# Kernel optimization log

Measured on AMD Instinct MI355X. Metric: run time of the kernel, lower is better.

## Reference

```python
import jax, jax.numpy as jnp
import numpy as np

N_NODES = 200000
N_EDGES = 6400000
N_GRAPHS = 1024
N_EMB = 1032
D = 16


def _gcn_conv(x, W, b, src, dst, n):
    # PyG GCNConv: h = x W; symmetric norm with self-loops; aggregate onto target (dst)
    h = x @ W
    deg = jax.ops.segment_sum(jnp.ones_like(dst, dtype=h.dtype), dst, num_segments=n) + 1.0
    dis = jax.lax.rsqrt(deg)
    norm = dis[src] * dis[dst]                      # [E]
    agg = jax.ops.segment_sum(h[src] * norm[:, None], dst, num_segments=n)
    agg = agg + h * (dis * dis)[:, None]            # self-loop term
    return agg + b


def _protein_embed(ids, edge_index, batch_ids, emb, W1, b1, W2, b2):
    n = ids.shape[0]
    x = emb[ids]                                    # embedding lookup [N, D]
    src, dst = edge_index[0], edge_index[1]
    h = jax.nn.relu(_gcn_conv(x, W1, b1, src, dst, n))
    h = _gcn_conv(h, W2, b2, src, dst, n)
    # global_mean_pool over graphs
    sums = jax.ops.segment_sum(h, batch_ids, num_segments=N_GRAPHS)
    cnt = jax.ops.segment_sum(jnp.ones((n,), h.dtype), batch_ids, num_segments=N_GRAPHS)
    return sums / jnp.maximum(cnt, 1.0)[:, None]    # [B, D]


def setup_inputs() -> dict:
    key = jax.random.key(0)
    ks = jax.random.split(key, 10)
    emb = jax.random.normal(ks[0], (N_EMB, D), jnp.float32) * 0.1
    W1 = jax.random.normal(ks[1], (D, D), jnp.float32) * (1.0 / np.sqrt(D))
    W2 = jax.random.normal(ks[2], (D, D), jnp.float32) * (1.0 / np.sqrt(D))
    fcW = jax.random.normal(ks[3], (6, 2 * D), jnp.float32) * (1.0 / np.sqrt(2 * D))
    b1 = jnp.zeros((D,), jnp.float32)
    b2 = jnp.zeros((D,), jnp.float32)
    fcb = jnp.zeros((6,), jnp.float32)
    rx = jax.random.randint(ks[4], (N_NODES,), 0, N_EMB)
    r_edge_index = jax.random.randint(ks[5], (2, N_EDGES), 0, N_NODES)
    r_batch = jnp.sort(jax.random.randint(ks[6], (N_NODES,), 0, N_GRAPHS))
    lx = jax.random.randint(ks[7], (N_NODES,), 0, N_EMB)
    l_edge_index = jax.random.randint(ks[8], (2, N_EDGES), 0, N_NODES)
    l_batch = jnp.sort(jax.random.randint(ks[9], (N_NODES,), 0, N_GRAPHS))
    return {"emb": emb, "W1": W1, "b1": b1, "W2": W2, "b2": b2, "fcW": fcW, "fcb": fcb,
            "rx": rx, "r_edge_index": r_edge_index, "r_batch": r_batch,
            "lx": lx, "l_edge_index": l_edge_index, "l_batch": l_batch}


def reference(emb, W1, b1, W2, b2, fcW, fcb, rx, r_edge_index, r_batch, lx, l_edge_index, l_batch):
    r = _protein_embed(rx, r_edge_index, r_batch, emb, W1, b1, W2, b2)
    l = _protein_embed(lx, l_edge_index, l_batch, emb, W1, b1, W2, b2)
    h = jnp.concatenate([r, l], axis=1)             # [B, 2D]
    out = h @ fcW.T + fcb                           # [B, 6]
    return out[:, :3], out[:, 3:]
```

## Files before the change

kernel.cpp:

```cpp
#include <hip/hip_runtime.h>
#include <hip/hip_bf16.h>

#define N_NODES 200000
#define N_GRAPHS 1024
#define D 16
#define NEDGE 6400000

#define BNODES 256
#define NBUK 782
#define NCH 512
#define ECHUNK 12500
#define EC4 (ECHUNK / 4)
#define OSTRIDE (NBUK + 1)
#define CAP 9216
#define GBLK 12500
#define GHALF 6250

__global__ __launch_bounds__(1024) void pA(
        const int* __restrict__ srcR, const int* __restrict__ dstR,
        const int* __restrict__ srcL, const int* __restrict__ dstL,
        unsigned int* __restrict__ slabC_R, unsigned int* __restrict__ slabC_L,
        int* __restrict__ offsT_R, int* __restrict__ offsT_L) {
    const int* src = blockIdx.y ? srcL : srcR;
    const int* dst = blockIdx.y ? dstL : dstR;
    unsigned int* slabC = blockIdx.y ? slabC_L : slabC_R;
    int* offsT = blockIdx.y ? offsT_L : offsT_R;

    __shared__ unsigned int stage[ECHUNK];
    __shared__ int lh[NBUK];
    __shared__ int lcur[NBUK];
    __shared__ int wsum[16];
    int t = threadIdx.x;
    int wave = t >> 6, lane = t & 63;
    int c = blockIdx.x;
    int base = c * ECHUNK;
    const int4* dst4 = (const int4*)(dst + base);
    const int4* src4 = (const int4*)(src + base);

    for (int k = t; k < NBUK; k += 1024) lh[k] = 0;
    __syncthreads();
    for (int i = t; i < EC4; i += 1024) {
        int4 d4 = dst4[i];
        atomicAdd(&lh[((unsigned int)d4.x) >> 8], 1);
        atomicAdd(&lh[((unsigned int)d4.y) >> 8], 1);
        atomicAdd(&lh[((unsigned int)d4.z) >> 8], 1);
        atomicAdd(&lh[((unsigned int)d4.w) >> 8], 1);
    }
    __syncthreads();

    int v = (t < NBUK) ? lh[t] : 0;
    int x = v;
#pragma unroll
    for (int d0 = 1; d0 < 64; d0 <<= 1) {
        int y = __shfl_up(x, d0, 64);
        if (lane >= d0) x += y;
    }
    if (lane == 63) wsum[wave] = x;
    __syncthreads();
    if (wave == 0 && lane < 16) {
        int s = wsum[lane];
#pragma unroll
        for (int d0 = 1; d0 < 16; d0 <<= 1) {
            int y = __shfl_up(s, d0, 64);
            if (lane >= d0) s += y;
        }
        wsum[lane] = s;
    }
    __syncthreads();
    int excl = x - v + (wave ? wsum[wave - 1] : 0);
    if (t < NBUK) lcur[t] = excl;
    __syncthreads();

    for (int i = t; i < EC4; i += 1024) {
        int4 d4 = dst4[i];
        int4 s4 = src4[i];
        int dd[4] = {d4.x, d4.y, d4.z, d4.w};
        int ss[4] = {s4.x, s4.y, s4.z, s4.w};
#pragma unroll
        for (int k = 0; k < 4; k++) {
            int pos = atomicAdd(&lcur[dd[k] >> 8], 1);
            stage[pos] = ((unsigned int)(dd[k] & 255) << 18) | (unsigned int)ss[k];
        }
    }
    __syncthreads();
    uint4* out4 = (uint4*)(slabC + base);
    const uint4* st4 = (const uint4*)stage;
    for (int i = t; i < EC4; i += 1024) out4[i] = st4[i];
    if (t < NBUK) offsT[c * OSTRIDE + t] = excl;
    if (t == 0) offsT[c * OSTRIDE + NBUK] = ECHUNK;
}

__global__ __launch_bounds__(256) void tr_kernel(
        const int* __restrict__ offsT_R, const int* __restrict__ offsT_L,
        int* __restrict__ offsTT_R, int* __restrict__ offsTT_L) {
    const int* in = blockIdx.z ? offsT_L : offsT_R;
    int* outp = blockIdx.z ? offsTT_L : offsTT_R;
    __shared__ int tile[32][33];
    int lx = threadIdx.x & 31, ly = threadIdx.x >> 5;
#pragma unroll
    for (int r = 0; r < 32; r += 8) {
        int row = blockIdx.y * 32 + ly + r;
        int col = blockIdx.x * 32 + lx;
        if (col < OSTRIDE) tile[ly + r][lx] = in[row * OSTRIDE + col];
    }
    __syncthreads();
#pragma unroll
    for (int r = 0; r < 32; r += 8) {
        int orow = blockIdx.x * 32 + ly + r;
        int ocol = blockIdx.y * 32 + lx;
        if (orow < OSTRIDE) outp[orow * NCH + ocol] = tile[lx][ly + r];
    }
}

__global__ __launch_bounds__(256) void pB(
        const unsigned int* __restrict__ slabC_R, const unsigned int* __restrict__ slabC_L,
        const int* __restrict__ offsTT_R, const int* __restrict__ offsTT_L,
        unsigned int* __restrict__ slabR, unsigned int* __restrict__ slabL,
        int2* __restrict__ metaR, int2* __restrict__ metaL,
        float* __restrict__ disR, float* __restrict__ disL) {
    int y = blockIdx.y;
    const unsigned int* slabC = y ? slabC_L : slabC_R;
    const int* offsTT = y ? offsTT_L : offsTT_R;
    unsigned int* slab = y ? slabL : slabR;
    int2* meta = y ? metaL : metaR;
    float* dis = y ? disL : disR;

    __shared__ unsigned int sin_[CAP];
    __shared__ int hcnt[BNODES], hoff[BNODES], hcur[BNODES];
    __shared__ int wtot[4];
    __shared__ int totc;
    int t = threadIdx.x;
    int lane = t & 63, wave = t >> 6;
    int b = blockIdx.x;

    int a0 = offsTT[b * NCH + t],        e0 = offsTT[(b + 1) * NCH + t];
    int a1 = offsTT[b * NCH + t + 256],  e1 = offsTT[(b + 1) * NCH + t + 256];
    int len = (e0 - a0) + (e1 - a1);

    int x = len;
#pragma unroll
    for (int d0 = 1; d0 < 64; d0 <<= 1) {
        int yy = __shfl_up(x, d0, 64);
        if (lane >= d0) x += yy;
    }
    if (lane == 63) wtot[wave] = x;
    hcnt[t] = 0;
    __syncthreads();
    int pre = 0;
    for (int w2 = 0; w2 < wave; w2++) pre += wtot[w2];
    int sbase = x - len + pre;
    if (t == 255) totc = sbase + len;
    __syncthreads();

    int p = sbase;
    {
        int cb = t * ECHUNK;
        for (int i = (a0 & ~3); i < e0; i += 4) {
            uint4 v = *(const uint4*)(slabC + cb + i);
            unsigned int vv[4] = {v.x, v.y, v.z, v.w};
#pragma unroll
            for (int k = 0; k < 4; k++) {
                int idx = i + k;
                if (idx >= a0 && idx < e0) { if (p < CAP) sin_[p] = vv[k]; p++; }
            }
        }
        cb = (t + 256) * ECHUNK;
        for (int i = (a1 & ~3); i < e1; i += 4) {
            uint4 v = *(const uint4*)(slabC + cb + i);
            unsigned int vv[4] = {v.x, v.y, v.z, v.w};
#pragma unroll
            for (int k = 0; k < 4; k++) {
                int idx = i + k;
                if (idx >= a1 && idx < e1) { if (p < CAP) sin_[p] = vv[k]; p++; }
            }
        }
    }
    __syncthreads();
    int cnt = totc;
    if (cnt > CAP) cnt = CAP;

    for (int i = t; i < cnt; i += 256) atomicAdd(&hcnt[sin_[i] >> 18], 1);
    __syncthreads();

    int v2 = hcnt[t];
    int x2 = v2;
#pragma unroll
    for (int d0 = 1; d0 < 64; d0 <<= 1) {
        int yy = __shfl_up(x2, d0, 64);
        if (lane >= d0) x2 += yy;
    }
    if (lane == 63) wtot[wave] = x2;
    __syncthreads();
    int pre2 = 0;
    for (int w2 = 0; w2 < wave; w2++) pre2 += wtot[w2];
    int ex = x2 - v2 + pre2;
    hoff[t] = ex;
    hcur[t] = ex;
    __syncthreads();

    int gb = b * CAP;
    for (int i = t; i < cnt; i += 256) {
        unsigned int r = sin_[i];
        int pp = atomicAdd(&hcur[r >> 18], 1);
        if (pp < CAP) slab[gb + pp] = r & 0x3FFFFu;
    }
    int node = (b << 8) + t;
    if (node < N_NODES) {
        meta[node] = make_int2(gb + hoff[t], gb + hoff[t] + hcnt[t]);
        dis[node] = rsqrtf((float)hcnt[t] + 1.0f);
    }
}

__global__ __launch_bounds__(256) void t1_kernel(
        const int* __restrict__ idsR, const int* __restrict__ idsL,
        const float* __restrict__ emb, const float* __restrict__ W,
        const float* __restrict__ disR, const float* __restrict__ disL,
        __hip_bfloat16* __restrict__ hsR, __hip_bfloat16* __restrict__ hsL) {
    int y = blockIdx.y;
    const int* ids = y ? idsL : idsR;
    const float* dis = y ? disL : disR;
    __hip_bfloat16* hs = y ? hsL : hsR;
    __shared__ float sW[D][D];
    __shared__ float sx[16][D + 1];
    int t = threadIdx.x;
    int j = t & 15, g = t >> 4;
    sW[g][j] = W[t];
    int i = (blockIdx.x << 4) + g;
    sx[g][j] = emb[(size_t)ids[i] * D + j];
    __syncthreads();
    float acc = 0.f;
#pragma unroll
    for (int k = 0; k < D; k++) acc += sx[g][k] * sW[k][j];
    hs[(size_t)i * D + j] = __float2bfloat16(acc * dis[i]);
}

__global__ __launch_bounds__(256) void g1_kernel(
        const int2* __restrict__ metaR, const int2* __restrict__ metaL,
        const unsigned int* __restrict__ csrR, const unsigned int* __restrict__ csrL,
        const __hip_bfloat16* __restrict__ hs1R, const __hip_bfloat16* __restrict__ hs1L,
        const float* __restrict__ disR, const float* __restrict__ disL,
        const float* __restrict__ b1, const float* __restrict__ W2,
        __hip_bfloat16* __restrict__ hs2R, __hip_bfloat16* __restrict__ hs2L) {
    int half = (blockIdx.x >= GHALF);
    int bx = blockIdx.x - (half ? GHALF : 0);
    const int2* meta = half ? metaL : metaR;
    const unsigned int* csr = half ? csrL : csrR;
    const __hip_bfloat16* hs1 = half ? hs1L : hs1R;
    const float* dis = half ? disL : disR;
    __hip_bfloat16* hs2 = half ? hs2L : hs2R;

    __shared__ float sW[D][D];
    __shared__ float sx[32][D + 1];
    int t = threadIdx.x;
    int jp = t & 7, g = t >> 3;
    sW[t >> 4][t & 15] = W2[t];
    int i = (bx << 5) + g;
    int2 be = meta[i];
    float2 acc = __bfloat1622float2(
        *(const __hip_bfloat162*)(hs1 + (size_t)i * D + 2 * jp));
    int e = be.x, end = be.y;
    for (; e + 8 <= end; e += 8) {
        int my = (int)csr[e + jp];
#pragma unroll
        for (int n = 0; n < 8; n++) {
            int s = __shfl(my, n, 8);
            float2 f = __bfloat1622float2(
                *(const __hip_bfloat162*)(hs1 + (size_t)s * D + 2 * jp));
            acc.x += f.x; acc.y += f.y;
        }
    }
    for (; e < end; e++) {
        int s = csr[e];
        float2 f = __bfloat1622float2(
            *(const __hip_bfloat162*)(hs1 + (size_t)s * D + 2 * jp));
        acc.x += f.x; acc.y += f.y;
    }
    float di = dis[i];
    sx[g][2 * jp]     = fmaxf(acc.x * di + b1[2 * jp], 0.f);
    sx[g][2 * jp + 1] = fmaxf(acc.y * di + b1[2 * jp + 1], 0.f);
    __syncthreads();
    float a0 = 0.f, a1 = 0.f;
#pragma unroll
    for (int k = 0; k < D; k++) {
        float xv = sx[g][k];
        a0 += xv * sW[k][2 * jp];
        a1 += xv * sW[k][2 * jp + 1];
    }
    *(__hip_bfloat162*)(hs2 + (size_t)i * D + 2 * jp) =
        __float22bfloat162_rn(make_float2(a0 * di, a1 * di));
}

__global__ __launch_bounds__(256) void g2_kernel(
        const int2* __restrict__ metaR, const int2* __restrict__ metaL,
        const unsigned int* __restrict__ csrR, const unsigned int* __restrict__ csrL,
        const __hip_bfloat16* __restrict__ hs2R, const __hip_bfloat16* __restrict__ hs2L,
        const float* __restrict__ disR, const float* __restrict__ disL,
        const float* __restrict__ b2,
        const int* __restrict__ batR, const int* __restrict__ batL,
        float* __restrict__ sumsR, float* __restrict__ sumsL,
        float* __restrict__ cntR, float* __restrict__ cntL) {
    int half = (blockIdx.x >= GHALF);
    int bx = blockIdx.x - (half ? GHALF : 0);
    const int2* meta = half ? metaL : metaR;
    const unsigned int* csr = half ? csrL : csrR;
    const __hip_bfloat16* hs2 = half ? hs2L : hs2R;
    const float* dis = half ? disL : disR;
    const int* batch = half ? batL : batR;
    float* sums = half ? sumsL : sumsR;
    float* cnt = half ? cntL : cntR;

    __shared__ float sv[32][D + 1];
    __shared__ int sb[32];
    int t = threadIdx.x;
    int jp = t & 7, g = t >> 3;
    int i = (bx << 5) + g;
    int2 be = meta[i];
    float2 acc = __bfloat1622float2(
        *(const __hip_bfloat162*)(hs2 + (size_t)i * D + 2 * jp));
    int e = be.x, end = be.y;
    for (; e + 8 <= end; e += 8) {
        int my = (int)csr[e + jp];
#pragma unroll
        for (int n = 0; n < 8; n++) {
            int s = __shfl(my, n, 8);
            float2 f = __bfloat1622float2(
                *(const __hip_bfloat162*)(hs2 + (size_t)s * D + 2 * jp));
            acc.x += f.x; acc.y += f.y;
        }
    }
    for (; e < end; e++) {
        int s = csr[e];
        float2 f = __bfloat1622float2(
            *(const __hip_bfloat162*)(hs2 + (size_t)s * D + 2 * jp));
        acc.x += f.x; acc.y += f.y;
    }
    float di = dis[i];
    int bi = batch[i];
    sv[g][2 * jp]     = acc.x * di + b2[2 * jp];
    sv[g][2 * jp + 1] = acc.y * di + b2[2 * jp + 1];
    if (jp == 0) sb[g] = bi;
    __syncthreads();
    bool runend = (g == 31) || (sb[g + 1] != bi);
    if (runend) {
        float s0 = 0.f, s1 = 0.f;
        int gg = g;
        while (gg >= 0 && sb[gg] == bi) { s0 += sv[gg][2 * jp]; s1 += sv[gg][2 * jp + 1]; gg--; }
        atomicAdd(&sums[bi * D + 2 * jp], s0);
        atomicAdd(&sums[bi * D + 2 * jp + 1], s1);
        if (jp == 0) atomicAdd(&cnt[bi], (float)(g - gg));
    }
}

__global__ void final_kernel(const float* __restrict__ rs, const float* __restrict__ rc,
                             const float* __restrict__ ls, const float* __restrict__ lc,
                             const float* __restrict__ fcW, const float* __restrict__ fcb,
                             float* __restrict__ out) {
    int b = blockIdx.x * blockDim.x + threadIdx.x;
    if (b >= N_GRAPHS) return;
    float hc[2 * D];
    float rn = fmaxf(rc[b], 1.f), ln = fmaxf(lc[b], 1.f);
#pragma unroll
    for (int j = 0; j < D; j++) {
        hc[j]     = rs[b * D + j] / rn;
        hc[D + j] = ls[b * D + j] / ln;
    }
#pragma unroll
    for (int c = 0; c < 6; c++) {
        float acc = fcb[c];
#pragma unroll
        for (int j = 0; j < 2 * D; j++) acc += hc[j] * fcW[c * 2 * D + j];
        if (c < 3) out[b * 3 + c] = acc;
        else       out[N_GRAPHS * 3 + b * 3 + (c - 3)] = acc;
    }
}

extern "C" void kernel_launch(void* const* d_in, const int* in_sizes, int n_in,
                              void* d_out, int out_size, void* d_ws, size_t ws_size,
                              hipStream_t stream) {
    const float* emb = (const float*)d_in[0];
    const float* W1  = (const float*)d_in[1];
    const float* b1  = (const float*)d_in[2];
    const float* W2  = (const float*)d_in[3];
    const float* b2  = (const float*)d_in[4];
    const float* fcW = (const float*)d_in[5];
    const float* fcb = (const float*)d_in[6];
    const int* rx = (const int*)d_in[7];
    const int* re = (const int*)d_in[8];
    const int* rb = (const int*)d_in[9];
    const int* lx = (const int*)d_in[10];
    const int* le = (const int*)d_in[11];
    const int* lb = (const int*)d_in[12];
    float* out = (float*)d_out;

    char* w = (char*)d_ws;
    unsigned int* slabC_R = (unsigned int*)w;
    __hip_bfloat16* hs1R = (__hip_bfloat16*)w;
    __hip_bfloat16* hs1L = hs1R + (size_t)N_NODES * D;
    __hip_bfloat16* hs2R = hs1L + (size_t)N_NODES * D;
    __hip_bfloat16* hs2L = hs2R + (size_t)N_NODES * D;
    w += (size_t)NEDGE * 4;
    unsigned int* slabC_L = (unsigned int*)w;  w += (size_t)NEDGE * 4;
    unsigned int* slabR = (unsigned int*)w;    w += (size_t)NBUK * CAP * 4;
    unsigned int* slabL = (unsigned int*)w;    w += (size_t)NBUK * CAP * 4;
    int* offsT_R = (int*)w;                    w += (size_t)NCH * OSTRIDE * 4;
    int* offsT_L = (int*)w;                    w += (size_t)NCH * OSTRIDE * 4;
    int* offsTT_R = (int*)w;                   w += (size_t)OSTRIDE * NCH * 4;
    int* offsTT_L = (int*)w;                   w += (size_t)OSTRIDE * NCH * 4;
    int2* metaR = (int2*)w;                    w += (size_t)N_NODES * 8;
    int2* metaL = (int2*)w;                    w += (size_t)N_NODES * 8;
    float* disR = (float*)w;                   w += (size_t)N_NODES * 4;
    float* disL = (float*)w;                   w += (size_t)N_NODES * 4;
    float* sums0 = (float*)w;                  w += (size_t)N_GRAPHS * D * 4;
    float* cnt0  = (float*)w;                  w += (size_t)N_GRAPHS * 4;
    float* sums1 = (float*)w;                  w += (size_t)N_GRAPHS * D * 4;
    float* cnt1  = (float*)w;                  w += (size_t)N_GRAPHS * 4;

    const int* srcR = re;  const int* dstR = re + NEDGE;
    const int* srcL = le;  const int* dstL = le + NEDGE;

    hipMemsetAsync(sums0, 0, ((size_t)N_GRAPHS * (D + 1)) * 2 * sizeof(float), stream);

    pA<<<dim3(NCH, 2), 1024, 0, stream>>>(srcR, dstR, srcL, dstL,
                                          slabC_R, slabC_L, offsT_R, offsT_L);
    tr_kernel<<<dim3((OSTRIDE + 31) / 32, NCH / 32, 2), 256, 0, stream>>>(
        offsT_R, offsT_L, offsTT_R, offsTT_L);
    pB<<<dim3(NBUK, 2), 256, 0, stream>>>(slabC_R, slabC_L, offsTT_R, offsTT_L,
                                          slabR, slabL, metaR, metaL, disR, disL);

    t1_kernel<<<dim3(GBLK, 2), 256, 0, stream>>>(rx, lx, emb, W1, disR, disL, hs1R, hs1L);
    g1_kernel<<<2 * GHALF, 256, 0, stream>>>(metaR, metaL, slabR, slabL,
                                             hs1R, hs1L, disR, disL, b1, W2, hs2R, hs2L);
    g2_kernel<<<2 * GHALF, 256, 0, stream>>>(metaR, metaL, slabR, slabL,
                                             hs2R, hs2L, disR, disL, b2, rb, lb,
                                             sums0, sums1, cnt0, cnt1);
    final_kernel<<<(N_GRAPHS + 255) / 256, 256, 0, stream>>>(
        sums0, cnt0, sums1, cnt1, fcW, fcb, out);
}
```

Measured before the change: 543.4 us.

## Split neighbor aggregation into two source-range passes for cache locality

Buckets each node's in-edges by whether the source index falls below or above a split point, storing three offsets per node. Each GCN aggregation becomes two kernels: the first gathers from the low half of node features and writes float2 partials, the second gathers from the high half and finishes the layer. The intent is to halve the random-gather working set per pass so it stays in cache, at the cost of an extra launch, partial-sum write/read traffic and a larger meta array.

```diff
diff --git a/kernel.cpp b/kernel.cpp
--- a/kernel.cpp
+++ b/kernel.cpp
@@ -5,6 +5,7 @@
 #define N_GRAPHS 1024
 #define D 16
 #define NEDGE 6400000
+#define SPLIT 100000
 
 #define BNODES 256
 #define NBUK 782
@@ -116,17 +117,17 @@
         const unsigned int* __restrict__ slabC_R, const unsigned int* __restrict__ slabC_L,
         const int* __restrict__ offsTT_R, const int* __restrict__ offsTT_L,
         unsigned int* __restrict__ slabR, unsigned int* __restrict__ slabL,
-        int2* __restrict__ metaR, int2* __restrict__ metaL,
+        int4* __restrict__ metaR, int4* __restrict__ metaL,
         float* __restrict__ disR, float* __restrict__ disL) {
     int y = blockIdx.y;
     const unsigned int* slabC = y ? slabC_L : slabC_R;
     const int* offsTT = y ? offsTT_L : offsTT_R;
     unsigned int* slab = y ? slabL : slabR;
-    int2* meta = y ? metaL : metaR;
+    int4* meta = y ? metaL : metaR;
     float* dis = y ? disL : disR;
 
     __shared__ unsigned int sin_[CAP];
-    __shared__ int hcnt[BNODES], hoff[BNODES], hcur[BNODES];
+    __shared__ int hcnt[2 * BNODES], hcur[2 * BNODES];
     __shared__ int wtot[4];
     __shared__ int totc;
     int t = threadIdx.x;
@@ -144,7 +145,8 @@
         if (lane >= d0) x += yy;
     }
     if (lane == 63) wtot[wave] = x;
-    hcnt[t] = 0;
+    hcnt[2 * t] = 0;
+    hcnt[2 * t + 1] = 0;
     __syncthreads();
     int pre = 0;
     for (int w2 = 0; w2 < wave; w2++) pre += wtot[w2];
@@ -179,11 +181,16 @@
     int cnt = totc;
     if (cnt > CAP) cnt = CAP;
 
-    for (int i = t; i < cnt; i += 256) atomicAdd(&hcnt[sin_[i] >> 18], 1);
-    __syncthreads();
-
-    int v2 = hcnt[t];
-    int x2 = v2;
+    for (int i = t; i < cnt; i += 256) {
+        unsigned int r = sin_[i];
+        int key = (int)((r >> 18) << 1) | (int)((r & 0x3FFFFu) >= (unsigned)SPLIT);
+        atomicAdd(&hcnt[key], 1);
+    }
+    __syncthreads();
+
+    int v0 = hcnt[2 * t], v1 = hcnt[2 * t + 1];
+    int len2 = v0 + v1;
+    int x2 = len2;
 #pragma unroll
     for (int d0 = 1; d0 < 64; d0 <<= 1) {
         int yy = __shfl_up(x2, d0, 64);
@@ -193,21 +200,22 @@
     __syncthreads();
     int pre2 = 0;
     for (int w2 = 0; w2 < wave; w2++) pre2 += wtot[w2];
-    int ex = x2 - v2 + pre2;
-    hoff[t] = ex;
-    hcur[t] = ex;
+    int ex = x2 - len2 + pre2;
+    hcur[2 * t] = ex;
+    hcur[2 * t + 1] = ex + v0;
     __syncthreads();
 
     int gb = b * CAP;
     for (int i = t; i < cnt; i += 256) {
         unsigned int r = sin_[i];
-        int pp = atomicAdd(&hcur[r >> 18], 1);
+        int key = (int)((r >> 18) << 1) | (int)((r & 0x3FFFFu) >= (unsigned)SPLIT);
+        int pp = atomicAdd(&hcur[key], 1);
         if (pp < CAP) slab[gb + pp] = r & 0x3FFFFu;
     }
     int node = (b << 8) + t;
     if (node < N_NODES) {
-        meta[node] = make_int2(gb + hoff[t], gb + hoff[t] + hcnt[t]);
-        dis[node] = rsqrtf((float)hcnt[t] + 1.0f);
+        meta[node] = make_int4(gb + ex, gb + ex + v0, gb + ex + v0 + v1, 0);
+        dis[node] = rsqrtf((float)(v0 + v1) + 1.0f);
     }
 }
 
@@ -234,19 +242,61 @@
     hs[(size_t)i * D + j] = __float2bfloat16(acc * dis[i]);
 }
 
-__global__ __launch_bounds__(256) void g1_kernel(
-        const int2* __restrict__ metaR, const int2* __restrict__ metaL,
+__global__ __launch_bounds__(256) void ga_kernel(
+        const int4* __restrict__ metaR, const int4* __restrict__ metaL,
+        const unsigned int* __restrict__ csrR, const unsigned int* __restrict__ csrL,
+        const __hip_bfloat16* __restrict__ hsR, const __hip_bfloat16* __restrict__ hsL,
+        float2* __restrict__ partR, float2* __restrict__ partL) {
+    int half = (blockIdx.x >= GHALF);
+    int bx = blockIdx.x - (half ? GHALF : 0);
+    const int4* meta = half ? metaL : metaR;
+    const unsigned int* csr = half ? csrL : csrR;
+    const __hip_bfloat16* hs = half ? hsL : hsR;
+    float2* part = half ? partL : partR;
+
+    int t = threadIdx.x;
+    int jp = t & 7, g = t >> 3;
+    int i = (bx << 5) + g;
+    int4 be = meta[i];
+    float2 acc = make_float2(0.f, 0.f);
+    if (i < SPLIT) {
+        acc = __bfloat1622float2(*(const __hip_bfloat162*)(hs + (size_t)i * D + 2 * jp));
+    }
+    int e = be.x, end = be.y;
+    for (; e + 8 <= end; e += 8) {
+        int my = (int)csr[e + jp];
+#pragma unroll
+        for (int n = 0; n < 8; n++) {
+            int s = __shfl(my, n, 8);
+            float2 f = __bfloat1622float2(
+                *(const __hip_bfloat162*)(hs + (size_t)s * D + 2 * jp));
+            acc.x += f.x; acc.y += f.y;
+        }
+    }
+    for (; e < end; e++) {
+        int s = (int)csr[e];
+        float2 f = __bfloat1622float2(
+            *(const __hip_bfloat162*)(hs + (size_t)s * D + 2 * jp));
+        acc.x += f.x; acc.y += f.y;
+    }
+    part[(size_t)i * 8 + jp] = acc;
+}
+
+__global__ __launch_bounds__(256) void g1b_kernel(
+        const int4* __restrict__ metaR, const int4* __restrict__ metaL,
         const unsigned int* __restrict__ csrR, const unsigned int* __restrict__ csrL,
         const __hip_bfloat16* __restrict__ hs1R, const __hip_bfloat16* __restrict__ hs1L,
         const float* __restrict__ disR, const float* __restrict__ disL,
         const float* __restrict__ b1, const float* __restrict__ W2,
+        const float2* __restrict__ partR, const float2* __restrict__ partL,
         __hip_bfloat16* __restrict__ hs2R, __hip_bfloat16* __restrict__ hs2L) {
     int half = (blockIdx.x >= GHALF);
     int bx = blockIdx.x - (half ? GHALF : 0);
-    const int2* meta = half ? metaL : metaR;
+    const int4* meta = half ? metaL : metaR;
     const unsigned int* csr = half ? csrL : csrR;
     const __hip_bfloat16* hs1 = half ? hs1L : hs1R;
     const float* dis = half ? disL : disR;
+    const float2* part = half ? partL : partR;
     __hip_bfloat16* hs2 = half ? hs2L : hs2R;
 
     __shared__ float sW[D][D];
@@ -255,10 +305,13 @@
     int jp = t & 7, g = t >> 3;
     sW[t >> 4][t & 15] = W2[t];
     int i = (bx << 5) + g;
-    int2 be = meta[i];
-    float2 acc = __bfloat1622float2(
-        *(const __hip_bfloat162*)(hs1 + (size_t)i * D + 2 * jp));
-    int e = be.x, end = be.y;
+    int4 be = meta[i];
+    float2 acc = part[(size_t)i * 8 + jp];
+    if (i >= SPLIT) {
+        float2 f = __bfloat1622float2(*(const __hip_bfloat162*)(hs1 + (size_t)i * D + 2 * jp));
+        acc.x += f.x; acc.y += f.y;
+    }
+    int e = be.y, end = be.z;
     for (; e + 8 <= end; e += 8) {
         int my = (int)csr[e + jp];
 #pragma unroll
@@ -270,7 +323,7 @@
         }
     }
     for (; e < end; e++) {
-        int s = csr[e];
+        int s = (int)csr[e];
         float2 f = __bfloat1622float2(
             *(const __hip_bfloat162*)(hs1 + (size_t)s * D + 2 * jp));
         acc.x += f.x; acc.y += f.y;
@@ -290,22 +343,24 @@
         __float22bfloat162_rn(make_float2(a0 * di, a1 * di));
 }
 
-__global__ __launch_bounds__(256) void g2_kernel(
-        const int2* __restrict__ metaR, const int2* __restrict__ metaL,
+__global__ __launch_bounds__(256) void g2b_kernel(
+        const int4* __restrict__ metaR, const int4* __restrict__ metaL,
         const unsigned int* __restrict__ csrR, const unsigned int* __restrict__ csrL,
         const __hip_bfloat16* __restrict__ hs2R, const __hip_bfloat16* __restrict__ hs2L,
         const float* __restrict__ disR, const float* __restrict__ disL,
         const float* __restrict__ b2,
         const int* __restrict__ batR, const int* __restrict__ batL,
+        const float2* __restrict__ partR, const float2* __restrict__ partL,
         float* __restrict__ sumsR, float* __restrict__ sumsL,
         float* __restrict__ cntR, float* __restrict__ cntL) {
     int half = (blockIdx.x >= GHALF);
     int bx = blockIdx.x - (half ? GHALF : 0);
-    const int2* meta = half ? metaL : metaR;
+    const int4* meta = half ? metaL : metaR;
     const unsigned int* csr = half ? csrL : csrR;
     const __hip_bfloat16* hs2 = half ? hs2L : hs2R;
     const float* dis = half ? disL : disR;
     const int* batch = half ? batL : batR;
+    const float2* part = half ? partL : partR;
     float* sums = half ? sumsL : sumsR;
     float* cnt = half ? cntL : cntR;
 
@@ -314,10 +369,13 @@
     int t = threadIdx.x;
     int jp = t & 7, g = t >> 3;
     int i = (bx << 5) + g;
-    int2 be = meta[i];
-    float2 acc = __bfloat1622float2(
-        *(const __hip_bfloat162*)(hs2 + (size_t)i * D + 2 * jp));
-    int e = be.x, end = be.y;
+    int4 be = meta[i];
+    float2 acc = part[(size_t)i * 8 + jp];
+    if (i >= SPLIT) {
+        float2 f = __bfloat1622float2(*(const __hip_bfloat162*)(hs2 + (size_t)i * D + 2 * jp));
+        acc.x += f.x; acc.y += f.y;
+    }
+    int e = be.y, end = be.z;
     for (; e + 8 <= end; e += 8) {
         int my = (int)csr[e + jp];
 #pragma unroll
@@ -329,7 +387,7 @@
         }
     }
     for (; e < end; e++) {
-        int s = csr[e];
+        int s = (int)csr[e];
         float2 f = __bfloat1622float2(
             *(const __hip_bfloat162*)(hs2 + (size_t)s * D + 2 * jp));
         acc.x += f.x; acc.y += f.y;
@@ -399,15 +457,18 @@
     __hip_bfloat16* hs2R = hs1L + (size_t)N_NODES * D;
     __hip_bfloat16* hs2L = hs2R + (size_t)N_NODES * D;
     w += (size_t)NEDGE * 4;
-    unsigned int* slabC_L = (unsigned int*)w;  w += (size_t)NEDGE * 4;
+    unsigned int* slabC_L = (unsigned int*)w;
+    float2* partR = (float2*)slabC_L;
+    float2* partL = partR + (size_t)N_NODES * 8;
+    w += (size_t)NEDGE * 4;
     unsigned int* slabR = (unsigned int*)w;    w += (size_t)NBUK * CAP * 4;
     unsigned int* slabL = (unsigned int*)w;    w += (size_t)NBUK * CAP * 4;
     int* offsT_R = (int*)w;                    w += (size_t)NCH * OSTRIDE * 4;
     int* offsT_L = (int*)w;                    w += (size_t)NCH * OSTRIDE * 4;
     int* offsTT_R = (int*)w;                   w += (size_t)OSTRIDE * NCH * 4;
     int* offsTT_L = (int*)w;                   w += (size_t)OSTRIDE * NCH * 4;
-    int2* metaR = (int2*)w;                    w += (size_t)N_NODES * 8;
-    int2* metaL = (int2*)w;                    w += (size_t)N_NODES * 8;
+    int4* metaR = (int4*)w;                    w += (size_t)N_NODES * 16;
+    int4* metaL = (int4*)w;                    w += (size_t)N_NODES * 16;
     float* disR = (float*)w;                   w += (size_t)N_NODES * 4;
     float* disL = (float*)w;                   w += (size_t)N_NODES * 4;
     float* sums0 = (float*)w;                  w += (size_t)N_GRAPHS * D * 4;
@@ -428,11 +489,16 @@
                                           slabR, slabL, metaR, metaL, disR, disL);
 
     t1_kernel<<<dim3(GBLK, 2), 256, 0, stream>>>(rx, lx, emb, W1, disR, disL, hs1R, hs1L);
-    g1_kernel<<<2 * GHALF, 256, 0, stream>>>(metaR, metaL, slabR, slabL,
-                                             hs1R, hs1L, disR, disL, b1, W2, hs2R, hs2L);
-    g2_kernel<<<2 * GHALF, 256, 0, stream>>>(metaR, metaL, slabR, slabL,
-                                             hs2R, hs2L, disR, disL, b2, rb, lb,
-                                             sums0, sums1, cnt0, cnt1);
+    ga_kernel<<<2 * GHALF, 256, 0, stream>>>(metaR, metaL, slabR, slabL,
+                                             hs1R, hs1L, partR, partL);
+    g1b_kernel<<<2 * GHALF, 256, 0, stream>>>(metaR, metaL, slabR, slabL,
+                                              hs1R, hs1L, disR, disL, b1, W2,
+                                              partR, partL, hs2R, hs2L);
+    ga_kernel<<<2 * GHALF, 256, 0, stream>>>(metaR, metaL, slabR, slabL,
+                                             hs2R, hs2L, partR, partL);
+    g2b_kernel<<<2 * GHALF, 256, 0, stream>>>(metaR, metaL, slabR, slabL,
+                                              hs2R, hs2L, disR, disL, b2, rb, lb,
+                                              partR, partL, sums0, sums1, cnt0, cnt1);
     final_kernel<<<(N_GRAPHS + 255) / 256, 256, 0, stream>>>(
         sums0, cnt0, sums1, cnt1, fcW, fcb, out);
 }
```

New measurement: 540.2 us. About the same (-0.6%).
